# Performance work log

Hardware: AMD Instinct MI355X
Metric: run time of the kernel (lower is better)

The kernel has to match this reference:

```python
import jax, jax.numpy as jnp
import numpy as np

H = 128
B = 512
T = 1024
FUT = 64


def setup_inputs() -> dict:
    key = jax.random.key(0)
    ks = jax.random.split(key, 11)
    k = 1.0 / np.sqrt(H)  # torch LSTMCell/Linear init range
    u = lambda kk, shape: jax.random.uniform(kk, shape, jnp.float32, -k, k)
    return {
        "x": jax.random.normal(ks[0], (B, T), jnp.float32),
        "W_ih1": u(ks[1], (4 * H, 1)),
        "b_ih1": u(ks[2], (4 * H,)),
        "W_hh1": u(ks[3], (4 * H, H)),
        "b_hh1": u(ks[4], (4 * H,)),
        "W_ih2": u(ks[5], (4 * H, H)),
        "b_ih2": u(ks[6], (4 * H,)),
        "W_hh2": u(ks[7], (4 * H, H)),
        "b_hh2": u(ks[8], (4 * H,)),
        "W_out": u(ks[9], (1, H)),
        "b_out": u(ks[10], (1,)),
        "future": FUT,
    }


def _cell(x_t, h, c, W_ih, b_ih, W_hh, b_hh):
    # torch.nn.LSTMCell: gates ordered i, f, g, o
    g = x_t @ W_ih.T + h @ W_hh.T + (b_ih + b_hh)
    i, f, gg, o = jnp.split(g, 4, axis=-1)
    c_new = jax.nn.sigmoid(f) * c + jax.nn.sigmoid(i) * jnp.tanh(gg)
    h_new = jax.nn.sigmoid(o) * jnp.tanh(c_new)
    return h_new, c_new


def reference(x, W_ih1, b_ih1, W_hh1, b_hh1, W_ih2, b_ih2, W_hh2, b_hh2, W_out, b_out, future):
    Bn = x.shape[0]
    Hn = W_hh1.shape[1]
    z = jnp.zeros((Bn, Hn), x.dtype)

    def enc_step(carry, x_t):
        h1, c1, h2, c2 = carry
        h1, c1 = _cell(x_t, h1, c1, W_ih1, b_ih1, W_hh1, b_hh1)
        h2, c2 = _cell(h1, h2, c2, W_ih2, b_ih2, W_hh2, b_hh2)
        return (h1, c1, h2, c2), None

    xs = x.T[:, :, None]  # [T, B, 1]
    (h1, c1, h2, c2), _ = jax.lax.scan(enc_step, (z, z, z, z), xs)
    out0 = h2 @ W_out.T + b_out  # [B, 1]

    def fut_step(carry, _):
        h1, c1, h2, c2, out = carry
        h1, c1 = _cell(out, h1, c1, W_ih1, b_ih1, W_hh1, b_hh1)
        h2, c2 = _cell(h1, h2, c2, W_ih2, b_ih2, W_hh2, b_hh2)
        out = h2 @ W_out.T + b_out
        return (h1, c1, h2, c2, out), out

    _, fouts = jax.lax.scan(fut_step, (h1, c1, h2, c2, out0), None, length=future - 1)
    # torch cats [B,1] tensors on dim=1 -> [B, future]
    return jnp.concatenate([out0, fouts[:, :, 0].T], axis=1)
```

## Files before the change

### kernel.cpp

```cpp
#include <hip/hip_runtime.h>

#define HH 128
#define TT 1024
#define NFUT 64
#define MB 2
#define NBLK 256
#define NITER (TT + NFUT - 1)

typedef _Float16 half8 __attribute__((ext_vector_type(8)));
typedef float floatx4 __attribute__((ext_vector_type(4)));

#define MFMA16(a, b, c) __builtin_amdgcn_mfma_f32_16x16x32_f16((a), (b), (c), 0, 0, 0)

__device__ __forceinline__ float sigm(float v) {
  return __builtin_amdgcn_rcpf(1.0f + __builtin_amdgcn_exp2f(v * -1.442695040888963f));
}
__device__ __forceinline__ float tanh_f(float v) {
  float a = __builtin_fabsf(v);
  float e = __builtin_amdgcn_exp2f(a * -2.885390081777927f);
  float r = (1.0f - e) * __builtin_amdgcn_rcpf(1.0f + e);
  return __builtin_copysignf(r, v);
}
__device__ __forceinline__ half8 ldw8(const float* __restrict__ p) {
  half8 r;
#pragma unroll
  for (int i = 0; i < 8; ++i) r[i] = (_Float16)p[i];
  return r;
}

__global__
__attribute__((amdgpu_flat_work_group_size(512, 512), amdgpu_waves_per_eu(2, 2)))
void lstm_kernel(
    const float* __restrict__ x,
    const float* __restrict__ W_ih1, const float* __restrict__ b_ih1,
    const float* __restrict__ W_hh1, const float* __restrict__ b_hh1,
    const float* __restrict__ W_ih2, const float* __restrict__ b_ih2,
    const float* __restrict__ W_hh2, const float* __restrict__ b_hh2,
    const float* __restrict__ W_out, const float* __restrict__ b_out,
    float* __restrict__ out)
{
  __shared__ __align__(16) _Float16 h1b[2][2048];
  __shared__ __align__(16) _Float16 h2b[2][2048];
  __shared__ __align__(16) _Float16 xs[TT * MB];
  __shared__ float opart[8 * MB];

  const int tid = (int)threadIdx.x;
  const int lane = tid & 63;
  const int w = tid >> 6;
  const int jl = lane & 15;
  const int rg = lane >> 4;
  const int j = w * 16 + jl;
  const int b0 = (int)blockIdx.x * MB;

  for (int idx = tid; idx < TT * MB; idx += 512) {
    int t = idx & (TT - 1);
    int bb = idx >> 10;
    xs[t * MB + bb] = (_Float16)x[(b0 + bb) * TT + t];
  }
  for (int idx = tid; idx < 2 * 2048; idx += 512) {
    h1b[idx >> 11][idx & 2047] = (_Float16)0.0f;
    h2b[idx >> 11][idx & 2047] = (_Float16)0.0f;
  }

  half8 A00, A01, A02, A03, A10, A11, A12, A13, A20, A21, A22, A23, A30, A31, A32, A33;
  half8 H00, H01, H02, H03, H10, H11, H12, H13, H20, H21, H22, H23, H30, H31, H32, H33;
  half8 I00, I01, I02, I03, I10, I11, I12, I13, I20, I21, I22, I23, I30, I31, I32, I33;
#define LDW(N, Q, P) do { \
    const float* _p = (P) + ((Q) * HH + j) * HH + rg * 8; \
    N##0 = ldw8(_p);      N##1 = ldw8(_p + 32); \
    N##2 = ldw8(_p + 64); N##3 = ldw8(_p + 96); } while (0)
  LDW(A0, 0, W_hh1); LDW(A1, 1, W_hh1); LDW(A2, 2, W_hh1); LDW(A3, 3, W_hh1);
  LDW(H0, 0, W_hh2); LDW(H1, 1, W_hh2); LDW(H2, 2, W_hh2); LDW(H3, 3, W_hh2);
  LDW(I0, 0, W_ih2); LDW(I1, 1, W_ih2); LDW(I2, 2, W_ih2); LDW(I3, 3, W_ih2);

  float bias1[4], bias2[4], wi1[4];
#pragma unroll
  for (int q = 0; q < 4; ++q) {
    bias1[q] = b_ih1[q * HH + j] + b_hh1[q * HH + j];
    bias2[q] = b_ih2[q * HH + j] + b_hh2[q * HH + j];
    wi1[q] = W_ih1[q * HH + j];
  }
  const float wo = W_out[j];
  const float bo = b_out[0];
  float c1 = 0.f, c2 = 0.f;

  __syncthreads();

  const int aoff = lane * 8;
  const int wbase = ((j >> 5) << 9) + (((j >> 3) & 3) << 7) + (j & 7) + (rg << 3);

#define G1K(KF) do { \
    half8 av = *(const half8*)(&h1b[cur][KF * 512 + aoff]); \
    acc0 = MFMA16(av, A0##KF, acc0); acc1 = MFMA16(av, A1##KF, acc1); \
    acc2 = MFMA16(av, A2##KF, acc2); acc3 = MFMA16(av, A3##KF, acc3); } while (0)
#define G2K(KF) do { \
    half8 av = *(const half8*)(&h2b[cur][KF * 512 + aoff]); \
    acc0 = MFMA16(av, H0##KF, acc0); acc1 = MFMA16(av, H1##KF, acc1); \
    acc2 = MFMA16(av, H2##KF, acc2); acc3 = MFMA16(av, H3##KF, acc3); \
    half8 aw = *(const half8*)(&h1b[nxt][KF * 512 + aoff]); \
    acc0 = MFMA16(aw, I0##KF, acc0); acc1 = MFMA16(aw, I1##KF, acc1); \
    acc2 = MFMA16(aw, I2##KF, acc2); acc3 = MFMA16(aw, I3##KF, acc3); } while (0)

  for (int i = 0; i < NITER; ++i) {
    const int cur = i & 1;
    const int nxt = cur ^ 1;

    float xv = 0.f;
    if (lane < 32) {
      if (i < TT) {
        xv = (float)xs[i * MB + rg];
      } else {
        float s = bo;
#pragma unroll
        for (int p8 = 0; p8 < 8; ++p8) s += opart[p8 * MB + rg];
        xv = s;
      }
    }

    floatx4 acc0 = {0.f,0.f,0.f,0.f}, acc1 = {0.f,0.f,0.f,0.f};
    floatx4 acc2 = {0.f,0.f,0.f,0.f}, acc3 = {0.f,0.f,0.f,0.f};
    G1K(0); G1K(1); G1K(2); G1K(3);
    {
      float t00 = __shfl(acc0[0], jl), t01 = __shfl(acc0[1], jl);
      float t10 = __shfl(acc1[0], jl), t11 = __shfl(acc1[1], jl);
      float t20 = __shfl(acc2[0], jl), t21 = __shfl(acc2[1], jl);
      float t30 = __shfl(acc3[0], jl), t31 = __shfl(acc3[1], jl);
      if (lane < 32) {
        float gi = ((lane & 16) ? t01 : t00) + xv * wi1[0] + bias1[0];
        float gf = ((lane & 16) ? t11 : t10) + xv * wi1[1] + bias1[1];
        float gg = ((lane & 16) ? t21 : t20) + xv * wi1[2] + bias1[2];
        float go = ((lane & 16) ? t31 : t30) + xv * wi1[3] + bias1[3];
        c1 = sigm(gf) * c1 + sigm(gi) * tanh_f(gg);
        float h = sigm(go) * tanh_f(c1);
        h1b[nxt][wbase] = (_Float16)h;
      }
    }
    __syncthreads();

    acc0 = (floatx4){0.f,0.f,0.f,0.f}; acc1 = (floatx4){0.f,0.f,0.f,0.f};
    acc2 = (floatx4){0.f,0.f,0.f,0.f}; acc3 = (floatx4){0.f,0.f,0.f,0.f};
    G2K(0); G2K(1); G2K(2); G2K(3);
    {
      float t00 = __shfl(acc0[0], jl), t01 = __shfl(acc0[1], jl);
      float t10 = __shfl(acc1[0], jl), t11 = __shfl(acc1[1], jl);
      float t20 = __shfl(acc2[0], jl), t21 = __shfl(acc2[1], jl);
      float t30 = __shfl(acc3[0], jl), t31 = __shfl(acc3[1], jl);
      if (lane < 32) {
        float gi = ((lane & 16) ? t01 : t00) + bias2[0];
        float gf = ((lane & 16) ? t11 : t10) + bias2[1];
        float gg = ((lane & 16) ? t21 : t20) + bias2[2];
        float go = ((lane & 16) ? t31 : t30) + bias2[3];
        c2 = sigm(gf) * c2 + sigm(gi) * tanh_f(gg);
        float h = sigm(go) * tanh_f(c2);
        h2b[nxt][wbase] = (_Float16)h;
        if (i >= TT - 1) {
          float p = h * wo;
          p += __shfl_xor(p, 1);
          p += __shfl_xor(p, 2);
          p += __shfl_xor(p, 4);
          p += __shfl_xor(p, 8);
          if (jl == 0) opart[w * MB + rg] = p;
        }
      }
    }
    __syncthreads();

    if (i >= TT - 1 && w == 0 && lane < MB) {
      float s = bo;
#pragma unroll
      for (int p8 = 0; p8 < 8; ++p8) s += opart[p8 * MB + lane];
      out[(b0 + lane) * NFUT + (i - (TT - 1))] = s;
    }
  }
}

extern "C" void kernel_launch(void* const* d_in, const int* in_sizes, int n_in,
                              void* d_out, int out_size, void* d_ws, size_t ws_size,
                              hipStream_t stream) {
  const float* x     = (const float*)d_in[0];
  const float* W_ih1 = (const float*)d_in[1];
  const float* b_ih1 = (const float*)d_in[2];
  const float* W_hh1 = (const float*)d_in[3];
  const float* b_hh1 = (const float*)d_in[4];
  const float* W_ih2 = (const float*)d_in[5];
  const float* b_ih2 = (const float*)d_in[6];
  const float* W_hh2 = (const float*)d_in[7];
  const float* b_hh2 = (const float*)d_in[8];
  const float* W_out = (const float*)d_in[9];
  const float* b_out = (const float*)d_in[10];
  (void)in_sizes; (void)n_in; (void)out_size; (void)d_ws; (void)ws_size;

  lstm_kernel<<<dim3(NBLK), dim3(512), 0, stream>>>(
      x, W_ih1, b_ih1, W_hh1, b_hh1, W_ih2, b_ih2, W_hh2, b_hh2, W_out, b_out,
      (float*)d_out);
}
```

Baseline: 1.695 ms.

## Drop per-step barrier in encoder, fold bias into MFMA accumulators, remove shuffles

The MFMA accumulators are now initialised with the bias and input-projection terms, so the separate adds after the matrix step go away. Each lane reads its gate values directly from accumulator rows 0 and 1 (the two batch elements), which removes the cross-lane shuffles; the cost is that every lane computes the activations redundantly and only lanes 0-15 store. The second __syncthreads per step is now executed only in the forecast phase, where outputs feed back as inputs. This relies on the double-buffered h1/h2 layout staying race-free with a single barrier per encoder step.

After: 2.631 ms. 1.55x slower.

```diff
diff --git a/kernel.cpp b/kernel.cpp
--- a/kernel.cpp
+++ b/kernel.cpp
@@ -50,12 +50,12 @@
   const int jl = lane & 15;
   const int rg = lane >> 4;
   const int j = w * 16 + jl;
-  const int b0 = (int)blockIdx.x * MB;
+  const int b0g = (int)blockIdx.x * MB;
 
   for (int idx = tid; idx < TT * MB; idx += 512) {
     int t = idx & (TT - 1);
     int bb = idx >> 10;
-    xs[t * MB + bb] = (_Float16)x[(b0 + bb) * TT + t];
+    xs[t * MB + bb] = (_Float16)x[(b0g + bb) * TT + t];
   }
   for (int idx = tid; idx < 2 * 2048; idx += 512) {
     h1b[idx >> 11][idx & 2047] = (_Float16)0.0f;
@@ -82,94 +82,97 @@
   }
   const float wo = W_out[j];
   const float bo = b_out[0];
-  float c1 = 0.f, c2 = 0.f;
+  float c1a = 0.f, c1b = 0.f, c2a = 0.f, c2b = 0.f;
 
   __syncthreads();
 
   const int aoff = lane * 8;
-  const int wbase = ((j >> 5) << 9) + (((j >> 3) & 3) << 7) + (j & 7) + (rg << 3);
+  const int wb = ((j >> 5) << 9) + (((j >> 3) & 3) << 7) + (j & 7);
 
 #define G1K(KF) do { \
     half8 av = *(const half8*)(&h1b[cur][KF * 512 + aoff]); \
-    acc0 = MFMA16(av, A0##KF, acc0); acc1 = MFMA16(av, A1##KF, acc1); \
-    acc2 = MFMA16(av, A2##KF, acc2); acc3 = MFMA16(av, A3##KF, acc3); } while (0)
+    a0 = MFMA16(av, A0##KF, a0); a1 = MFMA16(av, A1##KF, a1); \
+    a2 = MFMA16(av, A2##KF, a2); a3 = MFMA16(av, A3##KF, a3); } while (0)
 #define G2K(KF) do { \
     half8 av = *(const half8*)(&h2b[cur][KF * 512 + aoff]); \
-    acc0 = MFMA16(av, H0##KF, acc0); acc1 = MFMA16(av, H1##KF, acc1); \
-    acc2 = MFMA16(av, H2##KF, acc2); acc3 = MFMA16(av, H3##KF, acc3); \
+    g0 = MFMA16(av, H0##KF, g0); g1 = MFMA16(av, H1##KF, g1); \
+    g2 = MFMA16(av, H2##KF, g2); g3 = MFMA16(av, H3##KF, g3); \
     half8 aw = *(const half8*)(&h1b[nxt][KF * 512 + aoff]); \
-    acc0 = MFMA16(aw, I0##KF, acc0); acc1 = MFMA16(aw, I1##KF, acc1); \
-    acc2 = MFMA16(aw, I2##KF, acc2); acc3 = MFMA16(aw, I3##KF, acc3); } while (0)
+    g0 = MFMA16(aw, I0##KF, g0); g1 = MFMA16(aw, I1##KF, g1); \
+    g2 = MFMA16(aw, I2##KF, g2); g3 = MFMA16(aw, I3##KF, g3); } while (0)
 
   for (int i = 0; i < NITER; ++i) {
     const int cur = i & 1;
     const int nxt = cur ^ 1;
 
-    float xv = 0.f;
-    if (lane < 32) {
-      if (i < TT) {
-        xv = (float)xs[i * MB + rg];
-      } else {
-        float s = bo;
+    float x0, x1;
+    if (i < TT) {
+      x0 = (float)xs[i * MB + 0];
+      x1 = (float)xs[i * MB + 1];
+    } else {
+      float s0 = bo, s1 = bo;
 #pragma unroll
-        for (int p8 = 0; p8 < 8; ++p8) s += opart[p8 * MB + rg];
-        xv = s;
+      for (int p = 0; p < 8; ++p) {
+        s0 += opart[p * MB + 0];
+        s1 += opart[p * MB + 1];
       }
+      x0 = s0; x1 = s1;
     }
 
-    floatx4 acc0 = {0.f,0.f,0.f,0.f}, acc1 = {0.f,0.f,0.f,0.f};
-    floatx4 acc2 = {0.f,0.f,0.f,0.f}, acc3 = {0.f,0.f,0.f,0.f};
+    floatx4 a0, a1, a2, a3;
+    a0[0] = bias1[0] + x0 * wi1[0]; a0[1] = bias1[0] + x1 * wi1[0]; a0[2] = bias1[0]; a0[3] = bias1[0];
+    a1[0] = bias1[1] + x0 * wi1[1]; a1[1] = bias1[1] + x1 * wi1[1]; a1[2] = bias1[1]; a1[3] = bias1[1];
+    a2[0] = bias1[2] + x0 * wi1[2]; a2[1] = bias1[2] + x1 * wi1[2]; a2[2] = bias1[2]; a2[3] = bias1[2];
+    a3[0] = bias1[3] + x0 * wi1[3]; a3[1] = bias1[3] + x1 * wi1[3]; a3[2] = bias1[3]; a3[3] = bias1[3];
     G1K(0); G1K(1); G1K(2); G1K(3);
     {
-      float t00 = __shfl(acc0[0], jl), t01 = __shfl(acc0[1], jl);
-      float t10 = __shfl(acc1[0], jl), t11 = __shfl(acc1[1], jl);
-      float t20 = __shfl(acc2[0], jl), t21 = __shfl(acc2[1], jl);
-      float t30 = __shfl(acc3[0], jl), t31 = __shfl(acc3[1], jl);
-      if (lane < 32) {
-        float gi = ((lane & 16) ? t01 : t00) + xv * wi1[0] + bias1[0];
-        float gf = ((lane & 16) ? t11 : t10) + xv * wi1[1] + bias1[1];
-        float gg = ((lane & 16) ? t21 : t20) + xv * wi1[2] + bias1[2];
-        float go = ((lane & 16) ? t31 : t30) + xv * wi1[3] + bias1[3];
-        c1 = sigm(gf) * c1 + sigm(gi) * tanh_f(gg);
-        float h = sigm(go) * tanh_f(c1);
-        h1b[nxt][wbase] = (_Float16)h;
+      c1a = sigm(a1[0]) * c1a + sigm(a0[0]) * tanh_f(a2[0]);
+      c1b = sigm(a1[1]) * c1b + sigm(a0[1]) * tanh_f(a2[1]);
+      float h0 = sigm(a3[0]) * tanh_f(c1a);
+      float h1 = sigm(a3[1]) * tanh_f(c1b);
+      if (lane < 16) {
+        h1b[nxt][wb] = (_Float16)h0;
+        h1b[nxt][wb + 8] = (_Float16)h1;
       }
     }
     __syncthreads();
 
-    acc0 = (floatx4){0.f,0.f,0.f,0.f}; acc1 = (floatx4){0.f,0.f,0.f,0.f};
-    acc2 = (floatx4){0.f,0.f,0.f,0.f}; acc3 = (floatx4){0.f,0.f,0.f,0.f};
+    floatx4 g0, g1, g2, g3;
+    g0[0] = bias2[0]; g0[1] = bias2[0]; g0[2] = bias2[0]; g0[3] = bias2[0];
+    g1[0] = bias2[1]; g1[1] = bias2[1]; g1[2] = bias2[1]; g1[3] = bias2[1];
+    g2[0] = bias2[2]; g2[1] = bias2[2]; g2[2] = bias2[2]; g2[3] = bias2[2];
+    g3[0] = bias2[3]; g3[1] = bias2[3]; g3[2] = bias2[3]; g3[3] = bias2[3];
     G2K(0); G2K(1); G2K(2); G2K(3);
     {
-      float t00 = __shfl(acc0[0], jl), t01 = __shfl(acc0[1], jl);
-      float t10 = __shfl(acc1[0], jl), t11 = __shfl(acc1[1], jl);
-      float t20 = __shfl(acc2[0], jl), t21 = __shfl(acc2[1], jl);
-      float t30 = __shfl(acc3[0], jl), t31 = __shfl(acc3[1], jl);
-      if (lane < 32) {
-        float gi = ((lane & 16) ? t01 : t00) + bias2[0];
-        float gf = ((lane & 16) ? t11 : t10) + bias2[1];
-        float gg = ((lane & 16) ? t21 : t20) + bias2[2];
-        float go = ((lane & 16) ? t31 : t30) + bias2[3];
-        c2 = sigm(gf) * c2 + sigm(gi) * tanh_f(gg);
-        float h = sigm(go) * tanh_f(c2);
-        h2b[nxt][wbase] = (_Float16)h;
-        if (i >= TT - 1) {
-          float p = h * wo;
-          p += __shfl_xor(p, 1);
-          p += __shfl_xor(p, 2);
-          p += __shfl_xor(p, 4);
-          p += __shfl_xor(p, 8);
-          if (jl == 0) opart[w * MB + rg] = p;
+      c2a = sigm(g1[0]) * c2a + sigm(g0[0]) * tanh_f(g2[0]);
+      c2b = sigm(g1[1]) * c2b + sigm(g0[1]) * tanh_f(g2[1]);
+      float h0 = sigm(g3[0]) * tanh_f(c2a);
+      float h1 = sigm(g3[1]) * tanh_f(c2b);
+      if (lane < 16) {
+        h2b[nxt][wb] = (_Float16)h0;
+        h2b[nxt][wb + 8] = (_Float16)h1;
+      }
+      if (i >= TT - 1) {
+        float p0 = h0 * wo, p1 = h1 * wo;
+        p0 += __shfl_xor(p0, 1); p1 += __shfl_xor(p1, 1);
+        p0 += __shfl_xor(p0, 2); p1 += __shfl_xor(p1, 2);
+        p0 += __shfl_xor(p0, 4); p1 += __shfl_xor(p1, 4);
+        p0 += __shfl_xor(p0, 8); p1 += __shfl_xor(p1, 8);
+        if (lane == 0) {
+          opart[w * MB + 0] = p0;
+          opart[w * MB + 1] = p1;
         }
       }
     }
-    __syncthreads();
 
-    if (i >= TT - 1 && w == 0 && lane < MB) {
-      float s = bo;
+    if (i >= TT - 1) {
+      __syncthreads();
+      if (w == 0 && lane < MB) {
+        float s = bo;
 #pragma unroll
-      for (int p8 = 0; p8 < 8; ++p8) s += opart[p8 * MB + lane];
-      out[(b0 + lane) * NFUT + (i - (TT - 1))] = s;
+        for (int p = 0; p < 8; ++p) s += opart[p * MB + lane];
+        out[(b0g + lane) * NFUT + (i - (TT - 1))] = s;
+      }
     }
   }
 }
```

## Replace MFMA recurrent matvecs with packed fp16 dot2 per-lane reductions

Applied to the files above, without the earlier changes.

The per-step recurrent matrix-vector products move from 16x16x32 MFMA tiles, which were mostly padding for a batch of 2, to v_dot2 fp16 instructions. Each lane holds half of the K dimension for two gate rows and both batch elements, and partial sums are combined with cross-lane shuffles. This drops the shuffle-and-select extraction of MFMA outputs and uses compact h buffers in shared memory. The output write is folded into the start of the next iteration. In exchange the kernel issues many more VALU dot instructions, holds more weight registers per lane, and reads h through LDS broadcast loads.

New measurement: 2.637 ms. 1.56x slower.

```diff
diff --git a/kernel.cpp b/kernel.cpp
--- a/kernel.cpp
+++ b/kernel.cpp
@@ -5,12 +5,10 @@
 #define NFUT 64
 #define MB 2
 #define NBLK 256
-#define NITER (TT + NFUT - 1)
-
-typedef _Float16 half8 __attribute__((ext_vector_type(8)));
-typedef float floatx4 __attribute__((ext_vector_type(4)));
-
-#define MFMA16(a, b, c) __builtin_amdgcn_mfma_f32_16x16x32_f16((a), (b), (c), 0, 0, 0)
+
+typedef unsigned int u32;
+typedef u32 u32x4 __attribute__((ext_vector_type(4)));
+typedef _Float16 half2v __attribute__((ext_vector_type(2)));
 
 __device__ __forceinline__ float sigm(float v) {
   return __builtin_amdgcn_rcpf(1.0f + __builtin_amdgcn_exp2f(v * -1.442695040888963f));
@@ -21,12 +19,23 @@
   float r = (1.0f - e) * __builtin_amdgcn_rcpf(1.0f + e);
   return __builtin_copysignf(r, v);
 }
-__device__ __forceinline__ half8 ldw8(const float* __restrict__ p) {
-  half8 r;
-#pragma unroll
-  for (int i = 0; i < 8; ++i) r[i] = (_Float16)p[i];
+__device__ __forceinline__ u32 pk2(float a, float b) {
+  union { _Float16 h[2]; u32 u; } x;
+  x.h[0] = (_Float16)a; x.h[1] = (_Float16)b;
+  return x.u;
+}
+__device__ __forceinline__ u32x4 ldpk8(const float* __restrict__ p) {
+  u32x4 r;
+  r[0] = pk2(p[0], p[1]); r[1] = pk2(p[2], p[3]);
+  r[2] = pk2(p[4], p[5]); r[3] = pk2(p[6], p[7]);
   return r;
 }
+__device__ __forceinline__ float d2(u32 h, u32 w, float a) {
+  return __builtin_amdgcn_fdot2(__builtin_bit_cast(half2v, h),
+                                __builtin_bit_cast(half2v, w), a, false);
+}
+#define D8(A, H, W) do { A = d2(H[0], W[0], A); A = d2(H[1], W[1], A); \
+                         A = d2(H[2], W[2], A); A = d2(H[3], W[3], A); } while (0)
 
 __global__
 __attribute__((amdgpu_flat_work_group_size(512, 512), amdgpu_waves_per_eu(2, 2)))
@@ -39,138 +48,138 @@
     const float* __restrict__ W_out, const float* __restrict__ b_out,
     float* __restrict__ out)
 {
-  __shared__ __align__(16) _Float16 h1b[2][2048];
-  __shared__ __align__(16) _Float16 h2b[2][2048];
-  __shared__ __align__(16) _Float16 xs[TT * MB];
+  __shared__ __align__(16) _Float16 h1L[2][2][HH];
+  __shared__ __align__(16) _Float16 h2L[2][2][HH];
+  __shared__ float xs[TT * MB];
   __shared__ float opart[8 * MB];
 
   const int tid = (int)threadIdx.x;
   const int lane = tid & 63;
   const int w = tid >> 6;
-  const int jl = lane & 15;
-  const int rg = lane >> 4;
-  const int j = w * 16 + jl;
-  const int b0 = (int)blockIdx.x * MB;
+  const int ul = lane & 15;
+  const int kh = (lane >> 4) & 1;
+  const int gp = lane >> 5;
+  const int u = w * 16 + ul;
+  const int kh64 = kh * 64;
+  const int b0g = (int)blockIdx.x * MB;
 
   for (int idx = tid; idx < TT * MB; idx += 512) {
-    int t = idx & (TT - 1);
-    int bb = idx >> 10;
-    xs[t * MB + bb] = (_Float16)x[(b0 + bb) * TT + t];
+    int t = idx >> 1, b = idx & 1;
+    xs[idx] = x[(b0g + b) * TT + t];
   }
-  for (int idx = tid; idx < 2 * 2048; idx += 512) {
-    h1b[idx >> 11][idx & 2047] = (_Float16)0.0f;
-    h2b[idx >> 11][idx & 2047] = (_Float16)0.0f;
-  }
-
-  half8 A00, A01, A02, A03, A10, A11, A12, A13, A20, A21, A22, A23, A30, A31, A32, A33;
-  half8 H00, H01, H02, H03, H10, H11, H12, H13, H20, H21, H22, H23, H30, H31, H32, H33;
-  half8 I00, I01, I02, I03, I10, I11, I12, I13, I20, I21, I22, I23, I30, I31, I32, I33;
-#define LDW(N, Q, P) do { \
-    const float* _p = (P) + ((Q) * HH + j) * HH + rg * 8; \
-    N##0 = ldw8(_p);      N##1 = ldw8(_p + 32); \
-    N##2 = ldw8(_p + 64); N##3 = ldw8(_p + 96); } while (0)
-  LDW(A0, 0, W_hh1); LDW(A1, 1, W_hh1); LDW(A2, 2, W_hh1); LDW(A3, 3, W_hh1);
-  LDW(H0, 0, W_hh2); LDW(H1, 1, W_hh2); LDW(H2, 2, W_hh2); LDW(H3, 3, W_hh2);
-  LDW(I0, 0, W_ih2); LDW(I1, 1, W_ih2); LDW(I2, 2, W_ih2); LDW(I3, 3, W_ih2);
-
-  float bias1[4], bias2[4], wi1[4];
+  ((_Float16*)h1L)[tid] = (_Float16)0.0f;
+  ((_Float16*)h2L)[tid] = (_Float16)0.0f;
+
+  const int q0 = gp * 2, q1 = q0 + 1;
+  u32x4 W10_0,W10_1,W10_2,W10_3,W10_4,W10_5,W10_6,W10_7;
+  u32x4 W11_0,W11_1,W11_2,W11_3,W11_4,W11_5,W11_6,W11_7;
+  u32x4 W20_0,W20_1,W20_2,W20_3,W20_4,W20_5,W20_6,W20_7;
+  u32x4 W21_0,W21_1,W21_2,W21_3,W21_4,W21_5,W21_6,W21_7;
+  u32x4 W30_0,W30_1,W30_2,W30_3,W30_4,W30_5,W30_6,W30_7;
+  u32x4 W31_0,W31_1,W31_2,W31_3,W31_4,W31_5,W31_6,W31_7;
+#define LDALL(NM, MATP, Q) do { \
+    const float* _b = (MATP) + ((Q) * HH + u) * HH + kh64; \
+    NM##_0 = ldpk8(_b);      NM##_1 = ldpk8(_b + 8);  \
+    NM##_2 = ldpk8(_b + 16); NM##_3 = ldpk8(_b + 24); \
+    NM##_4 = ldpk8(_b + 32); NM##_5 = ldpk8(_b + 40); \
+    NM##_6 = ldpk8(_b + 48); NM##_7 = ldpk8(_b + 56); } while (0)
+  LDALL(W10, W_hh1, q0); LDALL(W11, W_hh1, q1);
+  LDALL(W20, W_hh2, q0); LDALL(W21, W_hh2, q1);
+  LDALL(W30, W_ih2, q0); LDALL(W31, W_ih2, q1);
+
+  float bias1v[4], bias2v[4], wi1v[4];
 #pragma unroll
   for (int q = 0; q < 4; ++q) {
-    bias1[q] = b_ih1[q * HH + j] + b_hh1[q * HH + j];
-    bias2[q] = b_ih2[q * HH + j] + b_hh2[q * HH + j];
-    wi1[q] = W_ih1[q * HH + j];
+    bias1v[q] = b_ih1[q * HH + u] + b_hh1[q * HH + u];
+    bias2v[q] = b_ih2[q * HH + u] + b_hh2[q * HH + u];
+    wi1v[q] = W_ih1[q * HH + u];
   }
-  const float wo = W_out[j];
+  const float wo = W_out[u];
   const float bo = b_out[0];
   float c1 = 0.f, c2 = 0.f;
 
   __syncthreads();
 
-  const int aoff = lane * 8;
-  const int wbase = ((j >> 5) << 9) + (((j >> 3) & 3) << 7) + (j & 7) + (rg << 3);
-
-#define G1K(KF) do { \
-    half8 av = *(const half8*)(&h1b[cur][KF * 512 + aoff]); \
-    acc0 = MFMA16(av, A0##KF, acc0); acc1 = MFMA16(av, A1##KF, acc1); \
-    acc2 = MFMA16(av, A2##KF, acc2); acc3 = MFMA16(av, A3##KF, acc3); } while (0)
-#define G2K(KF) do { \
-    half8 av = *(const half8*)(&h2b[cur][KF * 512 + aoff]); \
-    acc0 = MFMA16(av, H0##KF, acc0); acc1 = MFMA16(av, H1##KF, acc1); \
-    acc2 = MFMA16(av, H2##KF, acc2); acc3 = MFMA16(av, H3##KF, acc3); \
-    half8 aw = *(const half8*)(&h1b[nxt][KF * 512 + aoff]); \
-    acc0 = MFMA16(aw, I0##KF, acc0); acc1 = MFMA16(aw, I1##KF, acc1); \
-    acc2 = MFMA16(aw, I2##KF, acc2); acc3 = MFMA16(aw, I3##KF, acc3); } while (0)
-
-  for (int i = 0; i < NITER; ++i) {
-    const int cur = i & 1;
-    const int nxt = cur ^ 1;
-
-    float xv = 0.f;
-    if (lane < 32) {
-      if (i < TT) {
-        xv = (float)xs[i * MB + rg];
-      } else {
-        float s = bo;
-#pragma unroll
-        for (int p8 = 0; p8 < 8; ++p8) s += opart[p8 * MB + rg];
-        xv = s;
-      }
-    }
-
-    floatx4 acc0 = {0.f,0.f,0.f,0.f}, acc1 = {0.f,0.f,0.f,0.f};
-    floatx4 acc2 = {0.f,0.f,0.f,0.f}, acc3 = {0.f,0.f,0.f,0.f};
-    G1K(0); G1K(1); G1K(2); G1K(3);
-    {
-      float t00 = __shfl(acc0[0], jl), t01 = __shfl(acc0[1], jl);
-      float t10 = __shfl(acc1[0], jl), t11 = __shfl(acc1[1], jl);
-      float t20 = __shfl(acc2[0], jl), t21 = __shfl(acc2[1], jl);
-      float t30 = __shfl(acc3[0], jl), t31 = __shfl(acc3[1], jl);
-      if (lane < 32) {
-        float gi = ((lane & 16) ? t01 : t00) + xv * wi1[0] + bias1[0];
-        float gf = ((lane & 16) ? t11 : t10) + xv * wi1[1] + bias1[1];
-        float gg = ((lane & 16) ? t21 : t20) + xv * wi1[2] + bias1[2];
-        float go = ((lane & 16) ? t31 : t30) + xv * wi1[3] + bias1[3];
-        c1 = sigm(gf) * c1 + sigm(gi) * tanh_f(gg);
-        float h = sigm(go) * tanh_f(c1);
-        h1b[nxt][wbase] = (_Float16)h;
-      }
-    }
-    __syncthreads();
-
-    acc0 = (floatx4){0.f,0.f,0.f,0.f}; acc1 = (floatx4){0.f,0.f,0.f,0.f};
-    acc2 = (floatx4){0.f,0.f,0.f,0.f}; acc3 = (floatx4){0.f,0.f,0.f,0.f};
-    G2K(0); G2K(1); G2K(2); G2K(3);
-    {
-      float t00 = __shfl(acc0[0], jl), t01 = __shfl(acc0[1], jl);
-      float t10 = __shfl(acc1[0], jl), t11 = __shfl(acc1[1], jl);
-      float t20 = __shfl(acc2[0], jl), t21 = __shfl(acc2[1], jl);
-      float t30 = __shfl(acc3[0], jl), t31 = __shfl(acc3[1], jl);
-      if (lane < 32) {
-        float gi = ((lane & 16) ? t01 : t00) + bias2[0];
-        float gf = ((lane & 16) ? t11 : t10) + bias2[1];
-        float gg = ((lane & 16) ? t21 : t20) + bias2[2];
-        float go = ((lane & 16) ? t31 : t30) + bias2[3];
-        c2 = sigm(gf) * c2 + sigm(gi) * tanh_f(gg);
-        float h = sigm(go) * tanh_f(c2);
-        h2b[nxt][wbase] = (_Float16)h;
-        if (i >= TT - 1) {
-          float p = h * wo;
-          p += __shfl_xor(p, 1);
-          p += __shfl_xor(p, 2);
-          p += __shfl_xor(p, 4);
-          p += __shfl_xor(p, 8);
-          if (jl == 0) opart[w * MB + rg] = p;
-        }
-      }
-    }
-    __syncthreads();
-
-    if (i >= TT - 1 && w == 0 && lane < MB) {
+#define C1L(c) do { u32x4 H0 = hb0[c], H1 = hb1[c]; \
+    D8(a00, H0, W10_##c); D8(a10, H0, W11_##c); \
+    D8(a01, H1, W10_##c); D8(a11, H1, W11_##c); } while (0)
+#define C2L(c) do { u32x4 H0 = hb0[c], H1 = hb1[c]; \
+    D8(a00, H0, W20_##c); D8(a10, H0, W21_##c); \
+    D8(a01, H1, W20_##c); D8(a11, H1, W21_##c); } while (0)
+#define C3L(c) do { u32x4 H0 = jb0[c], H1 = jb1[c]; \
+    D8(a00, H0, W30_##c); D8(a10, H0, W31_##c); \
+    D8(a01, H1, W30_##c); D8(a11, H1, W31_##c); } while (0)
+#define COMBINE() \
+    a00 += __shfl_xor(a00, 16); a01 += __shfl_xor(a01, 16); \
+    a10 += __shfl_xor(a10, 16); a11 += __shfl_xor(a11, 16); \
+    float t0 = gp ? a00 : a01, t1 = gp ? a10 : a11; \
+    float o0 = __shfl_xor(t0, 32), o1 = __shfl_xor(t1, 32); \
+    float own0 = gp ? a01 : a00, own1 = gp ? a11 : a10; \
+    float gi = gp ? o0 : own0, gf = gp ? o1 : own1; \
+    float gg = gp ? own0 : o0, go = gp ? own1 : o1;
+
+  for (int k = 0; k < TT + NFUT; ++k) {
+    const int cur = k & 1;
+    const int prv = cur ^ 1;
+
+    float xb;
+    if (k < TT) {
+      xb = xs[k * MB + gp];
+    } else {
       float s = bo;
 #pragma unroll
-      for (int p8 = 0; p8 < 8; ++p8) s += opart[p8 * MB + lane];
-      out[(b0 + lane) * NFUT + (i - (TT - 1))] = s;
-    }
+      for (int p = 0; p < 8; ++p) s += opart[p * MB + gp];
+      xb = s;
+      if (w == 0 && (lane & 31) == 0) out[(b0g + gp) * NFUT + (k - TT)] = s;
+    }
+    if (k == TT + NFUT - 1) break;
+
+    float a00 = 0.f, a01 = 0.f, a10 = 0.f, a11 = 0.f;
+    {
+      const u32x4* hb0 = (const u32x4*)&h1L[prv][0][kh64];
+      const u32x4* hb1 = (const u32x4*)&h1L[prv][1][kh64];
+      C1L(0); C1L(1); C1L(2); C1L(3); C1L(4); C1L(5); C1L(6); C1L(7);
+    }
+    {
+      COMBINE();
+      gi += xb * wi1v[0] + bias1v[0];
+      gf += xb * wi1v[1] + bias1v[1];
+      gg += xb * wi1v[2] + bias1v[2];
+      go += xb * wi1v[3] + bias1v[3];
+      c1 = sigm(gf) * c1 + sigm(gi) * tanh_f(gg);
+      float h = sigm(go) * tanh_f(c1);
+      if (kh == 0) h1L[cur][gp][u] = (_Float16)h;
+    }
+    __syncthreads();
+
+    a00 = 0.f; a01 = 0.f; a10 = 0.f; a11 = 0.f;
+    {
+      const u32x4* hb0 = (const u32x4*)&h2L[prv][0][kh64];
+      const u32x4* hb1 = (const u32x4*)&h2L[prv][1][kh64];
+      C2L(0); C2L(1); C2L(2); C2L(3); C2L(4); C2L(5); C2L(6); C2L(7);
+      const u32x4* jb0 = (const u32x4*)&h1L[cur][0][kh64];
+      const u32x4* jb1 = (const u32x4*)&h1L[cur][1][kh64];
+      C3L(0); C3L(1); C3L(2); C3L(3); C3L(4); C3L(5); C3L(6); C3L(7);
+    }
+    {
+      COMBINE();
+      gi += bias2v[0];
+      gf += bias2v[1];
+      gg += bias2v[2];
+      go += bias2v[3];
+      c2 = sigm(gf) * c2 + sigm(gi) * tanh_f(gg);
+      float h = sigm(go) * tanh_f(c2);
+      if (kh == 0) h2L[cur][gp][u] = (_Float16)h;
+      if (k >= TT - 1) {
+        float p = h * wo;
+        p += __shfl_xor(p, 1);
+        p += __shfl_xor(p, 2);
+        p += __shfl_xor(p, 4);
+        p += __shfl_xor(p, 8);
+        if (ul == 0 && kh == 0) opart[w * MB + gp] = p;
+      }
+    }
+    __syncthreads();
   }
 }
 
```

## Drop per-step trailing barrier in encoder and cheapen gate shuffles

Applied to the files above, without the earlier changes.

The second __syncthreads per timestep now runs only during the future-prediction phase. The existing double buffering of h1b/h2b already orders the encoder steps, so one barrier per step is enough there. The eight indexed shuffles per gate stage become four xor-16 shuffles, and all 64 lanes compute the activations instead of a divergent half-wave. The first MFMA in each chain now takes a zero accumulator held in AGPRs instead of zeroing four accumulators every step. A sched_barrier stops the compiler from moving work across iterations. The risk is that this correctness argument about buffer reuse is subtle, and full-wave activation math doubles the transcendental work per wave.

After: 1.728 ms. Within noise of the previous version (+1.9%).

```diff
diff --git a/kernel.cpp b/kernel.cpp
--- a/kernel.cpp
+++ b/kernel.cpp
@@ -50,12 +50,12 @@
   const int jl = lane & 15;
   const int rg = lane >> 4;
   const int j = w * 16 + jl;
-  const int b0 = (int)blockIdx.x * MB;
+  const int b0g = (int)blockIdx.x * MB;
 
   for (int idx = tid; idx < TT * MB; idx += 512) {
     int t = idx & (TT - 1);
     int bb = idx >> 10;
-    xs[t * MB + bb] = (_Float16)x[(b0 + bb) * TT + t];
+    xs[t * MB + bb] = (_Float16)x[(b0g + bb) * TT + t];
   }
   for (int idx = tid; idx < 2 * 2048; idx += 512) {
     h1b[idx >> 11][idx & 2047] = (_Float16)0.0f;
@@ -84,93 +84,105 @@
   const float bo = b_out[0];
   float c1 = 0.f, c2 = 0.f;
 
+  floatx4 zc = {0.f, 0.f, 0.f, 0.f};
+  asm("" : "+a"(zc));
+
   __syncthreads();
 
   const int aoff = lane * 8;
-  const int wbase = ((j >> 5) << 9) + (((j >> 3) & 3) << 7) + (j & 7) + (rg << 3);
-
+  const int wb = ((j >> 5) << 9) + (((j >> 3) & 3) << 7) + (j & 7);
+  const int rowq = (lane >> 4) & 1;
+  const int wbR = wb + (rowq << 3);
+
+#define G1K0() do { \
+    half8 av = *(const half8*)(&h1b[cur][aoff]); \
+    p0 = MFMA16(av, A00, zc); p1 = MFMA16(av, A10, zc); \
+    p2 = MFMA16(av, A20, zc); p3 = MFMA16(av, A30, zc); } while (0)
 #define G1K(KF) do { \
     half8 av = *(const half8*)(&h1b[cur][KF * 512 + aoff]); \
-    acc0 = MFMA16(av, A0##KF, acc0); acc1 = MFMA16(av, A1##KF, acc1); \
-    acc2 = MFMA16(av, A2##KF, acc2); acc3 = MFMA16(av, A3##KF, acc3); } while (0)
+    p0 = MFMA16(av, A0##KF, p0); p1 = MFMA16(av, A1##KF, p1); \
+    p2 = MFMA16(av, A2##KF, p2); p3 = MFMA16(av, A3##KF, p3); } while (0)
+#define G2K0() do { \
+    half8 av = *(const half8*)(&h2b[cur][aoff]); \
+    p0 = MFMA16(av, H00, zc); p1 = MFMA16(av, H10, zc); \
+    p2 = MFMA16(av, H20, zc); p3 = MFMA16(av, H30, zc); \
+    half8 aw = *(const half8*)(&h1b[nxt][aoff]); \
+    p0 = MFMA16(aw, I00, p0); p1 = MFMA16(aw, I10, p1); \
+    p2 = MFMA16(aw, I20, p2); p3 = MFMA16(aw, I30, p3); } while (0)
 #define G2K(KF) do { \
     half8 av = *(const half8*)(&h2b[cur][KF * 512 + aoff]); \
-    acc0 = MFMA16(av, H0##KF, acc0); acc1 = MFMA16(av, H1##KF, acc1); \
-    acc2 = MFMA16(av, H2##KF, acc2); acc3 = MFMA16(av, H3##KF, acc3); \
+    p0 = MFMA16(av, H0##KF, p0); p1 = MFMA16(av, H1##KF, p1); \
+    p2 = MFMA16(av, H2##KF, p2); p3 = MFMA16(av, H3##KF, p3); \
     half8 aw = *(const half8*)(&h1b[nxt][KF * 512 + aoff]); \
-    acc0 = MFMA16(aw, I0##KF, acc0); acc1 = MFMA16(aw, I1##KF, acc1); \
-    acc2 = MFMA16(aw, I2##KF, acc2); acc3 = MFMA16(aw, I3##KF, acc3); } while (0)
+    p0 = MFMA16(aw, I0##KF, p0); p1 = MFMA16(aw, I1##KF, p1); \
+    p2 = MFMA16(aw, I2##KF, p2); p3 = MFMA16(aw, I3##KF, p3); } while (0)
 
   for (int i = 0; i < NITER; ++i) {
     const int cur = i & 1;
     const int nxt = cur ^ 1;
 
-    float xv = 0.f;
-    if (lane < 32) {
-      if (i < TT) {
-        xv = (float)xs[i * MB + rg];
-      } else {
+    float xb;
+    if (i < TT) {
+      xb = (float)xs[i * MB + rowq];
+    } else {
+      float s = bo;
+#pragma unroll
+      for (int p = 0; p < 8; ++p) s += opart[p * MB + rowq];
+      xb = s;
+    }
+
+    floatx4 p0, p1, p2, p3;
+    G1K0(); G1K(1); G1K(2); G1K(3);
+    {
+      float ri = __shfl_xor(p0[1], 16);
+      float rf = __shfl_xor(p1[1], 16);
+      float rgg = __shfl_xor(p2[1], 16);
+      float ro = __shfl_xor(p3[1], 16);
+      const bool hi = (lane & 16) != 0;
+      float gi = (hi ? ri : p0[0]) + xb * wi1[0] + bias1[0];
+      float gf = (hi ? rf : p1[0]) + xb * wi1[1] + bias1[1];
+      float gg = (hi ? rgg : p2[0]) + xb * wi1[2] + bias1[2];
+      float go = (hi ? ro : p3[0]) + xb * wi1[3] + bias1[3];
+      c1 = sigm(gf) * c1 + sigm(gi) * tanh_f(gg);
+      float h = sigm(go) * tanh_f(c1);
+      if (lane < 32) h1b[nxt][wbR] = (_Float16)h;
+    }
+    __syncthreads();
+
+    G2K0(); G2K(1); G2K(2); G2K(3);
+    {
+      float ri = __shfl_xor(p0[1], 16);
+      float rf = __shfl_xor(p1[1], 16);
+      float rgg = __shfl_xor(p2[1], 16);
+      float ro = __shfl_xor(p3[1], 16);
+      const bool hi = (lane & 16) != 0;
+      float gi = (hi ? ri : p0[0]) + bias2[0];
+      float gf = (hi ? rf : p1[0]) + bias2[1];
+      float gg = (hi ? rgg : p2[0]) + bias2[2];
+      float go = (hi ? ro : p3[0]) + bias2[3];
+      c2 = sigm(gf) * c2 + sigm(gi) * tanh_f(gg);
+      float h = sigm(go) * tanh_f(c2);
+      if (lane < 32) h2b[nxt][wbR] = (_Float16)h;
+      if (i >= TT - 1) {
+        float q = h * wo;
+        q += __shfl_xor(q, 1);
+        q += __shfl_xor(q, 2);
+        q += __shfl_xor(q, 4);
+        q += __shfl_xor(q, 8);
+        if ((lane & 15) == 0 && lane < 32) opart[w * MB + rowq] = q;
+      }
+    }
+
+    if (i >= TT - 1) {
+      __syncthreads();
+      if (w == 0 && (lane & 15) == 0 && lane < 32) {
         float s = bo;
 #pragma unroll
-        for (int p8 = 0; p8 < 8; ++p8) s += opart[p8 * MB + rg];
-        xv = s;
+        for (int p = 0; p < 8; ++p) s += opart[p * MB + rowq];
+        out[(b0g + rowq) * NFUT + (i - (TT - 1))] = s;
       }
     }
-
-    floatx4 acc0 = {0.f,0.f,0.f,0.f}, acc1 = {0.f,0.f,0.f,0.f};
-    floatx4 acc2 = {0.f,0.f,0.f,0.f}, acc3 = {0.f,0.f,0.f,0.f};
-    G1K(0); G1K(1); G1K(2); G1K(3);
-    {
-      float t00 = __shfl(acc0[0], jl), t01 = __shfl(acc0[1], jl);
-      float t10 = __shfl(acc1[0], jl), t11 = __shfl(acc1[1], jl);
-      float t20 = __shfl(acc2[0], jl), t21 = __shfl(acc2[1], jl);
-      float t30 = __shfl(acc3[0], jl), t31 = __shfl(acc3[1], jl);
-      if (lane < 32) {
-        float gi = ((lane & 16) ? t01 : t00) + xv * wi1[0] + bias1[0];
-        float gf = ((lane & 16) ? t11 : t10) + xv * wi1[1] + bias1[1];
-        float gg = ((lane & 16) ? t21 : t20) + xv * wi1[2] + bias1[2];
-        float go = ((lane & 16) ? t31 : t30) + xv * wi1[3] + bias1[3];
-        c1 = sigm(gf) * c1 + sigm(gi) * tanh_f(gg);
-        float h = sigm(go) * tanh_f(c1);
-        h1b[nxt][wbase] = (_Float16)h;
-      }
-    }
-    __syncthreads();
-
-    acc0 = (floatx4){0.f,0.f,0.f,0.f}; acc1 = (floatx4){0.f,0.f,0.f,0.f};
-    acc2 = (floatx4){0.f,0.f,0.f,0.f}; acc3 = (floatx4){0.f,0.f,0.f,0.f};
-    G2K(0); G2K(1); G2K(2); G2K(3);
-    {
-      float t00 = __shfl(acc0[0], jl), t01 = __shfl(acc0[1], jl);
-      float t10 = __shfl(acc1[0], jl), t11 = __shfl(acc1[1], jl);
-      float t20 = __shfl(acc2[0], jl), t21 = __shfl(acc2[1], jl);
-      float t30 = __shfl(acc3[0], jl), t31 = __shfl(acc3[1], jl);
-      if (lane < 32) {
-        float gi = ((lane & 16) ? t01 : t00) + bias2[0];
-        float gf = ((lane & 16) ? t11 : t10) + bias2[1];
-        float gg = ((lane & 16) ? t21 : t20) + bias2[2];
-        float go = ((lane & 16) ? t31 : t30) + bias2[3];
-        c2 = sigm(gf) * c2 + sigm(gi) * tanh_f(gg);
-        float h = sigm(go) * tanh_f(c2);
-        h2b[nxt][wbase] = (_Float16)h;
-        if (i >= TT - 1) {
-          float p = h * wo;
-          p += __shfl_xor(p, 1);
-          p += __shfl_xor(p, 2);
-          p += __shfl_xor(p, 4);
-          p += __shfl_xor(p, 8);
-          if (jl == 0) opart[w * MB + rg] = p;
-        }
-      }
-    }
-    __syncthreads();
-
-    if (i >= TT - 1 && w == 0 && lane < MB) {
-      float s = bo;
-#pragma unroll
-      for (int p8 = 0; p8 < 8; ++p8) s += opart[p8 * MB + lane];
-      out[(b0 + lane) * NFUT + (i - (TT - 1))] = s;
-    }
+    __builtin_amdgcn_sched_barrier(0);
   }
 }
 
```
